# Kernel optimization log

Measured on AMD Instinct MI355X. Metric: run time of the kernel, lower is better.

The kernel has to match this reference:

```python
import jax, jax.numpy as jnp
import numpy as np

PRIMES = [250007, 250013, 250027, 250031, 250037, 250043, 250049, 250051]
OFFSETS = np.concatenate([[0], np.cumsum(PRIMES)[:-1]]).astype(np.int64)  # [8]
TOTAL_ROWS = int(np.sum(PRIMES))
D_HEAD = 128          # embedding_dim_per_head
E_DIM = 8 * D_HEAD    # total_embedding_dim = 1024
H_DIM = 2560          # hidden_dim
KSIZE = 4             # causal depthwise conv kernel
EPS = 1e-6


def rmsnorm(x, g):
    # torch.nn.RMSNorm: x / sqrt(mean(x^2) + eps) * weight
    return x * jax.lax.rsqrt(jnp.mean(x * x, axis=-1, keepdims=True) + EPS) * g


def setup_inputs() -> dict:
    key = jax.random.key(0)
    ks = jax.random.split(key, 10)
    B, L = 4, 4096
    return {
        "hidden_states": jax.random.normal(ks[0], (B, L, H_DIM), jnp.float32),
        "engram_hash_indices": jax.random.randint(ks[1], (B, L, 8), 0, 250007, jnp.int64),
        "emb_table": jax.random.normal(ks[2], (TOTAL_ROWS, D_HEAD), jnp.float32) * 0.02,
        "w_v": jax.random.normal(ks[3], (H_DIM, E_DIM), jnp.float32) * 0.02,
        "w_k": jax.random.normal(ks[4], (H_DIM, E_DIM), jnp.float32) * 0.02,
        "g_h": jnp.ones((H_DIM,), jnp.float32),
        "g_k": jnp.ones((H_DIM,), jnp.float32),
        "g_v": jnp.ones((H_DIM,), jnp.float32),
        # paper zero-inits the conv; use small random weights so the conv path is exercised
        "conv_w": jax.random.normal(ks[5], (H_DIM, KSIZE), jnp.float32) * 0.02,
        "conv_b": jax.random.normal(ks[6], (H_DIM,), jnp.float32) * 0.02,
    }


def reference(hidden_states, engram_hash_indices, emb_table, w_v, w_k, g_h, g_k, g_v, conv_w, conv_b):
    B, L, H = hidden_states.shape
    # multi-head hash embedding retrieval
    idx = engram_hash_indices + jnp.asarray(OFFSETS)            # [B,L,8]
    e_t = emb_table[idx].reshape(B, L, E_DIM)                    # gather + concat heads
    # value / key projections (Linear, no bias)
    v_t = jnp.einsum('ble,he->blh', e_t, w_v)                    # [B,L,H]
    k_t = jnp.einsum('ble,he->blh', e_t, w_k)
    # context-aware gating
    h_n = rmsnorm(hidden_states, g_h)
    k_n = rmsnorm(k_t, g_k)
    dot = jnp.sum(h_n * k_n, axis=-1) / jnp.sqrt(jnp.float32(H))  # [B,L]
    stable = jnp.sqrt(jnp.maximum(jnp.abs(dot), 1e-6)) * jnp.sign(dot)
    alpha = jax.nn.sigmoid(stable)                               # [B,L]
    v_tilde = alpha[..., None] * v_t                             # [B,L,H]
    v_n = rmsnorm(v_tilde, g_v)
    # causal depthwise conv1d (left pad K-1) + SiLU
    x_pad = jnp.pad(v_n, ((0, 0), (KSIZE - 1, 0), (0, 0)))       # [B,L+3,H]
    conv = sum(conv_w[:, j] * x_pad[:, j:j + L, :] for j in range(KSIZE)) + conv_b
    y = jax.nn.silu(conv) + v_tilde
    return hidden_states + y
```

## Files before the change

kernel.cpp:

```cpp
#include <hip/hip_runtime.h>
#include <cstddef>
#include <cstdint>

typedef __bf16 bf16;
typedef __bf16 bf16x4 __attribute__((ext_vector_type(4)));
typedef __bf16 bf16x8 __attribute__((ext_vector_type(8)));
typedef float f32x4 __attribute__((ext_vector_type(4)));

#define AS1C(p) ((const __attribute__((address_space(1))) void*)(p))
#define AS3(p)  ((__attribute__((address_space(3))) void*)(p))

#define MROWS 16384
#define HDIM 2560
#define EDIM 1024
#define LSEQ 4096

static __device__ const int kHeadOff[8] = {0, 250007, 500020, 750047,
                                           1000078, 1250115, 1500158, 1750207};

__global__ __launch_bounds__(256) void k_gather(const int* __restrict__ hidx,
                                                const float* __restrict__ emb,
                                                bf16* __restrict__ E) {
  const int t = threadIdx.x;
  const int m = blockIdx.x * 2 + (t >> 7);
  const int tt = t & 127;
  const int head = tt >> 4;
  const int e8 = (tt & 15) * 8;
  const int rid = hidx[m * 8 + head] + kHeadOff[head];
  const float4 v0 = *(const float4*)(emb + (size_t)rid * 128 + e8);
  const float4 v1 = *(const float4*)(emb + (size_t)rid * 128 + e8 + 4);
  bf16x8 o;
  o[0] = (bf16)v0.x; o[1] = (bf16)v0.y; o[2] = (bf16)v0.z; o[3] = (bf16)v0.w;
  o[4] = (bf16)v1.x; o[5] = (bf16)v1.y; o[6] = (bf16)v1.z; o[7] = (bf16)v1.w;
  *(bf16x8*)(E + (size_t)m * EDIM + head * 128 + e8) = o;
}

__global__ __launch_bounds__(256) void k_cvt2(const float* __restrict__ s0,
                                              bf16* __restrict__ d0,
                                              const float* __restrict__ s1,
                                              bf16* __restrict__ d1) {
  int b = blockIdx.x;
  const float* src = s0;
  bf16* dst = d0;
  if (b >= 1280) { b -= 1280; src = s1; dst = d1; }
  const int i = (b * 256 + threadIdx.x) * 8;
  float4 a = *(const float4*)(src + i);
  float4 c = *(const float4*)(src + i + 4);
  bf16x8 o;
  o[0] = (bf16)a.x; o[1] = (bf16)a.y; o[2] = (bf16)a.z; o[3] = (bf16)a.w;
  o[4] = (bf16)c.x; o[5] = (bf16)c.y; o[6] = (bf16)c.z; o[7] = (bf16)c.w;
  *(bf16x8*)(dst + i) = o;
}

__device__ __forceinline__ float red16(float v) {
  v += __shfl_xor(v, 1);
  v += __shfl_xor(v, 2);
  v += __shfl_xor(v, 4);
  v += __shfl_xor(v, 8);
  return v;
}


#define LDSB 24576

__global__ __launch_bounds__(512, 4) void k_gemm(const bf16* __restrict__ A,
                                                 const bf16* __restrict__ Wv,
                                                 const bf16* __restrict__ Wk,
                                                 const float* __restrict__ hidden,
                                                 const float* __restrict__ g_h,
                                                 const float* __restrict__ g_k,
                                                 bf16* __restrict__ Vt,
                                                 float* __restrict__ S) {
  __shared__ __attribute__((aligned(16))) char ldsc[3 * LDSB];
  const int tid = threadIdx.x;
  const int wid = tid >> 6, lane = tid & 63;
  const int wm = wid >> 1, wn = wid & 1;
  const int r16 = lane & 15, khalf = lane >> 4;

  const int w = blockIdx.x;
  const int xcd = w & 7;
  const int r_ = w >> 3;
  const int gx = r_ >> 3;
  const int y = xcd * 8 + (r_ & 7);
  const int m0 = y * 256;
  const bool isV = (gx < 20);
  const int n0 = (isV ? gx : gx - 20) * 128;
  const bf16* Wp = isV ? Wv : Wk;

  const int sw = ((r16 >> 1) & 3) << 4;
  const int c0 = (khalf * 16) ^ sw;
  const int aRd = (wm * 64 + r16) * 64 + c0;
  const int bRd = 16384 + (wn * 64 + r16) * 64 + c0;

  const int srow = tid >> 2;
  const int scol = (((tid & 3) ^ ((tid >> 3) & 3))) * 8;
  const bf16* pA0 = A + (size_t)(m0 + srow) * EDIM + scol;
  const bf16* pA1 = pA0 + (size_t)128 * EDIM;
  const bf16* pB = Wp + (size_t)(n0 + srow) * EDIM + scol;
  const int ldsW = wid * 1024;

  f32x4 acc[4][4] = {};

#define STAGE(BUFO, KT) do {                                                   \
    __builtin_amdgcn_global_load_lds(AS1C(pA0 + (KT) * 32),                    \
        AS3(ldsc + (BUFO) + ldsW), 16, 0, 0);                                  \
    __builtin_amdgcn_global_load_lds(AS1C(pA1 + (KT) * 32),                    \
        AS3(ldsc + (BUFO) + 8192 + ldsW), 16, 0, 0);                           \
    __builtin_amdgcn_global_load_lds(AS1C(pB + (KT) * 32),                     \
        AS3(ldsc + (BUFO) + 16384 + ldsW), 16, 0, 0);                          \
    __builtin_amdgcn_sched_barrier(0);                                         \
  } while (0)

#define PHASE(BUFO, STBUF, KT, ST, VMW) do {                                   \
    if (ST) STAGE(STBUF, (KT) + 2);                                            \
    bf16x8 aF[4], bF[4];                                                       \
    _Pragma("unroll") for (int mi = 0; mi < 4; ++mi)                           \
      aF[mi] = *(const bf16x8*)(ldsc + (BUFO) + aRd + mi * 1024);              \
    _Pragma("unroll") for (int nj = 0; nj < 4; ++nj)                           \
      bF[nj] = *(const bf16x8*)(ldsc + (BUFO) + bRd + nj * 1024);              \
    __builtin_amdgcn_s_setprio(1);                                             \
    _Pragma("unroll") for (int nj = 0; nj < 4; ++nj)                           \
      _Pragma("unroll") for (int mi = 0; mi < 4; ++mi)                         \
        acc[mi][nj] = __builtin_amdgcn_mfma_f32_16x16x32_bf16(                 \
            aF[mi], bF[nj], acc[mi][nj], 0, 0, 0);                             \
    __builtin_amdgcn_s_setprio(0);                                             \
    asm volatile("s_waitcnt " VMW " lgkmcnt(0)" ::: "memory");                 \
    __builtin_amdgcn_s_barrier();                                              \
  } while (0)

  STAGE(0, 0);
  STAGE(LDSB, 1);
  asm volatile("s_waitcnt vmcnt(3)" ::: "memory");
  __builtin_amdgcn_s_barrier();

  for (int p = 0; p < 30; p += 3) {
    PHASE(0,        2 * LDSB, p,     true, "vmcnt(3)");
    PHASE(LDSB,     0,        p + 1, true, "vmcnt(3)");
    PHASE(2 * LDSB, LDSB,     p + 2, true, "vmcnt(3)");
  }
  PHASE(0, 0, 30, false, "vmcnt(0)");
  PHASE(LDSB, 0, 31, false, "");

  float* P = (float*)ldsc;
  if (isV) {
#pragma unroll
    for (int mi = 0; mi < 4; ++mi) {
#pragma unroll
      for (int nj = 0; nj < 4; ++nj) {
        const int col = n0 + wn * 64 + nj * 16 + r16;
#pragma unroll
        for (int r = 0; r < 4; ++r) {
          const int row = m0 + wm * 64 + mi * 16 + khalf * 4 + r;
          Vt[(size_t)row * HDIM + col] = (bf16)acc[mi][nj][r];
        }
      }
#pragma unroll
      for (int r = 0; r < 4; ++r) {
        float p = 0.f;
#pragma unroll
        for (int nj = 0; nj < 4; ++nj) p += acc[mi][nj][r] * acc[mi][nj][r];
        p = red16(p);
        if (r16 == 0) {
          const int rl = wm * 64 + mi * 16 + khalf * 4 + r;
          P[wn * 256 + rl] = p;
        }
      }
    }
    __syncthreads();
    if (tid < 256) {
      const float s = P[tid] + P[256 + tid];
      atomicAdd(&S[(size_t)(m0 + tid) * 4 + 3], s);
    }
  } else {
    float ghk[4];
#pragma unroll
    for (int nj = 0; nj < 4; ++nj) {
      const int col = n0 + wn * 64 + nj * 16 + r16;
      ghk[nj] = g_h[col] * g_k[col];
    }
#pragma unroll
    for (int mi = 0; mi < 4; ++mi) {
#pragma unroll
      for (int r = 0; r < 4; ++r) {
        const int row = m0 + wm * 64 + mi * 16 + khalf * 4 + r;
        float p1 = 0.f, p2 = 0.f, p3 = 0.f;
#pragma unroll
        for (int nj = 0; nj < 4; ++nj) {
          const int col = n0 + wn * 64 + nj * 16 + r16;
          const float k = acc[mi][nj][r];
          const float h = hidden[(size_t)row * HDIM + col];
          p1 += h * h;
          p2 += h * ghk[nj] * k;
          p3 += k * k;
        }
        p1 = red16(p1); p2 = red16(p2); p3 = red16(p3);
        if (r16 == 0) {
          const int rl = wm * 64 + mi * 16 + khalf * 4 + r;
          float* Pr = P + (wn * 256 + rl) * 3;
          Pr[0] = p1; Pr[1] = p2; Pr[2] = p3;
        }
      }
    }
    __syncthreads();
    for (int j = tid; j < 768; j += 512) {
      const int rl = j / 3, c = j % 3;
      const float s = P[j] + P[768 + j];
      atomicAdd(&S[(size_t)(m0 + rl) * 4 + c], s);
    }
  }
#undef STAGE
#undef PHASE
}

__device__ __forceinline__ void row_scal(const float* __restrict__ S, int m,
                                         float& alpha, float& av) {
  const float4 s = *(const float4*)(S + (size_t)m * 4);
  const float inv_h = rsqrtf(s.x * (1.f / HDIM) + 1e-6f);
  const float inv_k = rsqrtf(s.z * (1.f / HDIM) + 1e-6f);
  const float dot = s.y * inv_h * inv_k * 0.019764235f;
  float st = sqrtf(fmaxf(fabsf(dot), 1e-6f));
  st = (dot < 0.f) ? -st : st;
  if (dot == 0.f) st = 0.f;
  alpha = 1.f / (1.f + __expf(-st));
  av = alpha * rsqrtf(alpha * alpha * s.w * (1.f / HDIM) + 1e-6f);
}

__global__ __launch_bounds__(320) void k_fuse(const float* __restrict__ hidden,
                                              const bf16* __restrict__ Vt,
                                              const float* __restrict__ S,
                                              const float* __restrict__ g_v,
                                              const float* __restrict__ conv_w,
                                              const float* __restrict__ conv_b,
                                              float* __restrict__ out) {
  const int mbase = blockIdx.x * 8;
  const int l0 = mbase & (LSEQ - 1);
  const int t = threadIdx.x;
  const int h0 = t * 8;

  float gv[8], cb[8];
  *(float4*)&gv[0] = *(const float4*)(g_v + h0);
  *(float4*)&gv[4] = *(const float4*)(g_v + h0 + 4);
  *(float4*)&cb[0] = *(const float4*)(conv_b + h0);
  *(float4*)&cb[4] = *(const float4*)(conv_b + h0 + 4);
  float4 cw[8];
#pragma unroll
  for (int i = 0; i < 8; ++i)
    cw[i] = *(const float4*)(conv_w + (size_t)(h0 + i) * 4);

  float win[4][8];
#pragma unroll
  for (int jj = 0; jj < 4; ++jj)
#pragma unroll
    for (int i = 0; i < 8; ++i) win[jj][i] = 0.f;

#pragma unroll
  for (int j = 0; j < 11; ++j) {
    const int lj = l0 - 3 + j;
    const int m = mbase - 3 + j;
    float vtl[8];
    if (lj >= 0) {
      float alpha, av;
      row_scal(S, m, alpha, av);
      const bf16x8 v = *(const bf16x8*)(Vt + (size_t)m * HDIM + h0);
#pragma unroll
      for (int i = 0; i < 8; ++i) {
        const float vt = (float)v[i];
        vtl[i] = alpha * vt;
        win[j & 3][i] = av * vt * gv[i];
      }
    } else {
#pragma unroll
      for (int i = 0; i < 8; ++i) { win[j & 3][i] = 0.f; vtl[i] = 0.f; }
    }
    if (j >= 3) {
      const int R = mbase + j - 3;
      const size_t base = (size_t)R * HDIM + h0;
      float hx[8];
      *(float4*)&hx[0] = *(const float4*)(hidden + base);
      *(float4*)&hx[4] = *(const float4*)(hidden + base + 4);
      float o[8];
#pragma unroll
      for (int i = 0; i < 8; ++i) {
        float c = cb[i];
        c += ((const float*)&cw[i])[0] * win[(j - 3) & 3][i];
        c += ((const float*)&cw[i])[1] * win[(j - 2) & 3][i];
        c += ((const float*)&cw[i])[2] * win[(j - 1) & 3][i];
        c += ((const float*)&cw[i])[3] * win[j & 3][i];
        const float y = c / (1.f + __expf(-c));
        o[i] = hx[i] + y + vtl[i];
      }
      *(float4*)(out + base) = *(float4*)&o[0];
      *(float4*)(out + base + 4) = *(float4*)&o[4];
    }
  }
}

extern "C" void kernel_launch(void* const* d_in, const int* in_sizes, int n_in,
                              void* d_out, int out_size, void* d_ws,
                              size_t ws_size, hipStream_t stream) {
  const float* hidden = (const float*)d_in[0];
  const int* hashidx = (const int*)d_in[1];
  const float* emb = (const float*)d_in[2];
  const float* w_v = (const float*)d_in[3];
  const float* w_k = (const float*)d_in[4];
  const float* g_h = (const float*)d_in[5];
  const float* g_k = (const float*)d_in[6];
  const float* g_v = (const float*)d_in[7];
  const float* conv_w = (const float*)d_in[8];
  const float* conv_b = (const float*)d_in[9];
  float* out = (float*)d_out;

  char* w = (char*)d_ws;
  bf16* e16 = (bf16*)w;  w += (size_t)MROWS * EDIM * 2;
  bf16* wv16 = (bf16*)w; w += (size_t)HDIM * EDIM * 2;
  bf16* wk16 = (bf16*)w; w += (size_t)HDIM * EDIM * 2;
  bf16* vt16 = (bf16*)w; w += (size_t)MROWS * HDIM * 2;
  float* S = (float*)w;  w += (size_t)MROWS * 4 * 4;

  hipMemsetAsync(S, 0, (size_t)MROWS * 4 * 4, stream);
  k_gather<<<MROWS / 2, 256, 0, stream>>>(hashidx, emb, e16);
  k_cvt2<<<2560, 256, 0, stream>>>(w_v, wv16, w_k, wk16);
  k_gemm<<<dim3(2560), 512, 0, stream>>>(e16, wv16, wk16, hidden, g_h, g_k,
                                         vt16, S);
  k_fuse<<<MROWS / 8, 320, 0, stream>>>(hidden, vt16, S, g_v, conv_w, conv_b,
                                        out);
}
```

Before: 329.7 us.

## Fuse prep kernels and memset, switch GEMM to double buffering with XCD-aware tile mapping

Merges the gather, weight conversion and S-zeroing memset into a single launch, which removes two kernel launches and a memset. The GEMM goes from a triple-buffered LDS pipeline to a double-buffered one that stages each buffer right after it is consumed. This cuts LDS per block, which may allow more resident blocks. The block-to-tile mapping changes so that each XCD owns a group of N columns across all M rows, meant to improve L2 reuse of weight tiles. The shallower prefetch depth risks exposing more global load latency.

```diff
diff --git a/kernel.cpp b/kernel.cpp
--- a/kernel.cpp
+++ b/kernel.cpp
@@ -3,7 +3,6 @@
 #include <cstdint>
 
 typedef __bf16 bf16;
-typedef __bf16 bf16x4 __attribute__((ext_vector_type(4)));
 typedef __bf16 bf16x8 __attribute__((ext_vector_type(8)));
 typedef float f32x4 __attribute__((ext_vector_type(4)));
 
@@ -18,38 +17,44 @@
 static __device__ const int kHeadOff[8] = {0, 250007, 500020, 750047,
                                            1000078, 1250115, 1500158, 1750207};
 
-__global__ __launch_bounds__(256) void k_gather(const int* __restrict__ hidx,
-                                                const float* __restrict__ emb,
-                                                bf16* __restrict__ E) {
+__global__ __launch_bounds__(256) void k_prep(const int* __restrict__ hidx,
+                                              const float* __restrict__ emb,
+                                              bf16* __restrict__ E,
+                                              const float* __restrict__ wv,
+                                              bf16* __restrict__ wv16,
+                                              const float* __restrict__ wk,
+                                              bf16* __restrict__ wk16,
+                                              float* __restrict__ S) {
+  const int b = blockIdx.x;
   const int t = threadIdx.x;
-  const int m = blockIdx.x * 2 + (t >> 7);
-  const int tt = t & 127;
-  const int head = tt >> 4;
-  const int e8 = (tt & 15) * 8;
-  const int rid = hidx[m * 8 + head] + kHeadOff[head];
-  const float4 v0 = *(const float4*)(emb + (size_t)rid * 128 + e8);
-  const float4 v1 = *(const float4*)(emb + (size_t)rid * 128 + e8 + 4);
-  bf16x8 o;
-  o[0] = (bf16)v0.x; o[1] = (bf16)v0.y; o[2] = (bf16)v0.z; o[3] = (bf16)v0.w;
-  o[4] = (bf16)v1.x; o[5] = (bf16)v1.y; o[6] = (bf16)v1.z; o[7] = (bf16)v1.w;
-  *(bf16x8*)(E + (size_t)m * EDIM + head * 128 + e8) = o;
-}
-
-__global__ __launch_bounds__(256) void k_cvt2(const float* __restrict__ s0,
-                                              bf16* __restrict__ d0,
-                                              const float* __restrict__ s1,
-                                              bf16* __restrict__ d1) {
-  int b = blockIdx.x;
-  const float* src = s0;
-  bf16* dst = d0;
-  if (b >= 1280) { b -= 1280; src = s1; dst = d1; }
-  const int i = (b * 256 + threadIdx.x) * 8;
-  float4 a = *(const float4*)(src + i);
-  float4 c = *(const float4*)(src + i + 4);
-  bf16x8 o;
-  o[0] = (bf16)a.x; o[1] = (bf16)a.y; o[2] = (bf16)a.z; o[3] = (bf16)a.w;
-  o[4] = (bf16)c.x; o[5] = (bf16)c.y; o[6] = (bf16)c.z; o[7] = (bf16)c.w;
-  *(bf16x8*)(dst + i) = o;
+  if (b < 8192) {
+    const int m = b * 2 + (t >> 7);
+    const int tt = t & 127;
+    const int head = tt >> 4;
+    const int e8 = (tt & 15) * 8;
+    const int rid = hidx[m * 8 + head] + kHeadOff[head];
+    const float4 v0 = *(const float4*)(emb + (size_t)rid * 128 + e8);
+    const float4 v1 = *(const float4*)(emb + (size_t)rid * 128 + e8 + 4);
+    bf16x8 o;
+    o[0] = (bf16)v0.x; o[1] = (bf16)v0.y; o[2] = (bf16)v0.z; o[3] = (bf16)v0.w;
+    o[4] = (bf16)v1.x; o[5] = (bf16)v1.y; o[6] = (bf16)v1.z; o[7] = (bf16)v1.w;
+    *(bf16x8*)(E + (size_t)m * EDIM + head * 128 + e8) = o;
+  } else if (b < 10752) {
+    int bb = b - 8192;
+    const float* src = wv;
+    bf16* dst = wv16;
+    if (bb >= 1280) { bb -= 1280; src = wk; dst = wk16; }
+    const int i = (bb * 256 + t) * 8;
+    const float4 a = *(const float4*)(src + i);
+    const float4 c = *(const float4*)(src + i + 4);
+    bf16x8 o;
+    o[0] = (bf16)a.x; o[1] = (bf16)a.y; o[2] = (bf16)a.z; o[3] = (bf16)a.w;
+    o[4] = (bf16)c.x; o[5] = (bf16)c.y; o[6] = (bf16)c.z; o[7] = (bf16)c.w;
+    *(bf16x8*)(dst + i) = o;
+  } else {
+    const int i = ((b - 10752) * 256 + t) * 4;
+    *(float4*)(S + i) = float4{0.f, 0.f, 0.f, 0.f};
+  }
 }
 
 __device__ __forceinline__ float red16(float v) {
@@ -71,7 +76,7 @@
                                                  const float* __restrict__ g_k,
                                                  bf16* __restrict__ Vt,
                                                  float* __restrict__ S) {
-  __shared__ __attribute__((aligned(16))) char ldsc[3 * LDSB];
+  __shared__ __attribute__((aligned(16))) char ldsc[2 * LDSB];
   const int tid = threadIdx.x;
   const int wid = tid >> 6, lane = tid & 63;
   const int wm = wid >> 1, wn = wid & 1;
@@ -79,10 +84,11 @@
 
   const int w = blockIdx.x;
   const int xcd = w & 7;
-  const int r_ = w >> 3;
-  const int gx = r_ >> 3;
-  const int y = xcd * 8 + (r_ & 7);
-  const int m0 = y * 256;
+  const int s = w >> 3;
+  const int yy = s / 5;
+  const int gg = s % 5;
+  const int gx = xcd * 5 + gg;
+  const int m0 = yy * 256;
   const bool isV = (gx < 20);
   const int n0 = (isV ? gx : gx - 20) * 128;
   const bf16* Wp = isV ? Wv : Wk;
@@ -111,8 +117,7 @@
     __builtin_amdgcn_sched_barrier(0);                                         \
   } while (0)
 
-#define PHASE(BUFO, STBUF, KT, ST, VMW) do {                                   \
-    if (ST) STAGE(STBUF, (KT) + 2);                                            \
+#define PHASE_CORE(BUFO) do {                                                  \
     bf16x8 aF[4], bF[4];                                                       \
     _Pragma("unroll") for (int mi = 0; mi < 4; ++mi)                           \
       aF[mi] = *(const bf16x8*)(ldsc + (BUFO) + aRd + mi * 1024);              \
@@ -124,22 +129,37 @@
         acc[mi][nj] = __builtin_amdgcn_mfma_f32_16x16x32_bf16(                 \
             aF[mi], bF[nj], acc[mi][nj], 0, 0, 0);                             \
     __builtin_amdgcn_s_setprio(0);                                             \
-    asm volatile("s_waitcnt " VMW " lgkmcnt(0)" ::: "memory");                 \
+    asm volatile("s_waitcnt lgkmcnt(0)" ::: "memory");                         \
     __builtin_amdgcn_s_barrier();                                              \
   } while (0)
 
+#define BEGIN3() do {                                                          \
+    asm volatile("s_waitcnt vmcnt(3)" ::: "memory");                           \
+    __builtin_amdgcn_s_barrier();                                              \
+    asm volatile("" ::: "memory");                                             \
+  } while (0)
+
+#define BEGIN0() do {                                                          \
+    asm volatile("s_waitcnt vmcnt(0)" ::: "memory");                           \
+    __builtin_amdgcn_s_barrier();                                              \
+    asm volatile("" ::: "memory");                                             \
+  } while (0)
+
   STAGE(0, 0);
   STAGE(LDSB, 1);
-  asm volatile("s_waitcnt vmcnt(3)" ::: "memory");
-  __builtin_amdgcn_s_barrier();
-
-  for (int p = 0; p < 30; p += 3) {
-    PHASE(0,        2 * LDSB, p,     true, "vmcnt(3)");
-    PHASE(LDSB,     0,        p + 1, true, "vmcnt(3)");
-    PHASE(2 * LDSB, LDSB,     p + 2, true, "vmcnt(3)");
+
+  for (int p = 0; p < 30; p += 2) {
+    BEGIN3();
+    PHASE_CORE(0);
+    STAGE(0, p + 2);
+    BEGIN3();
+    PHASE_CORE(LDSB);
+    STAGE(LDSB, p + 3);
   }
-  PHASE(0, 0, 30, false, "vmcnt(0)");
-  PHASE(LDSB, 0, 31, false, "");
+  BEGIN3();
+  PHASE_CORE(0);
+  BEGIN0();
+  PHASE_CORE(LDSB);
 
   float* P = (float*)ldsc;
   if (isV) {
@@ -168,8 +188,8 @@
     }
     __syncthreads();
     if (tid < 256) {
-      const float s = P[tid] + P[256 + tid];
-      atomicAdd(&S[(size_t)(m0 + tid) * 4 + 3], s);
+      const float s2 = P[tid] + P[256 + tid];
+      atomicAdd(&S[(size_t)(m0 + tid) * 4 + 3], s2);
     }
   } else {
     float ghk[4];
@@ -204,12 +224,14 @@
     __syncthreads();
     for (int j = tid; j < 768; j += 512) {
       const int rl = j / 3, c = j % 3;
-      const float s = P[j] + P[768 + j];
-      atomicAdd(&S[(size_t)(m0 + rl) * 4 + c], s);
+      const float s2 = P[j] + P[768 + j];
+      atomicAdd(&S[(size_t)(m0 + rl) * 4 + c], s2);
     }
   }
 #undef STAGE
-#undef PHASE
+#undef PHASE_CORE
+#undef BEGIN3
+#undef BEGIN0
 }
 
 __device__ __forceinline__ void row_scal(const float* __restrict__ S, int m,
@@ -317,9 +339,7 @@
   bf16* vt16 = (bf16*)w; w += (size_t)MROWS * HDIM * 2;
   float* S = (float*)w;  w += (size_t)MROWS * 4 * 4;
 
-  hipMemsetAsync(S, 0, (size_t)MROWS * 4 * 4, stream);
-  k_gather<<<MROWS / 2, 256, 0, stream>>>(hashidx, emb, e16);
-  k_cvt2<<<2560, 256, 0, stream>>>(w_v, wv16, w_k, wk16);
+  k_prep<<<10816, 256, 0, stream>>>(hashidx, emb, e16, w_v, wv16, w_k, wk16, S);
   k_gemm<<<dim3(2560), 512, 0, stream>>>(e16, wv16, wk16, hidden, g_h, g_k,
                                          vt16, S);
   k_fuse<<<MROWS / 8, 320, 0, stream>>>(hidden, vt16, S, g_v, conv_w, conv_b,
```

Result: slower. 361.3 us (+9.6%).
